# Kernel tuning notes

Hardware: AMD Instinct MI355X
Metric: run time of the kernel (lower is better)

## Reference

```python
import jax, jax.numpy as jnp
import numpy as np

C = 256
CQK = C // 8  # reduction_ratio = 8


def setup_inputs() -> dict:
    key = jax.random.key(0)
    ks = jax.random.split(key, 8)
    B, H, W = 8, 64, 64
    x = jax.random.normal(ks[0], (B, C, H, W), dtype=jnp.float32)
    s_in = 1.0 / np.sqrt(C)
    Wq = jax.random.normal(ks[1], (CQK, C), dtype=jnp.float32) * s_in
    bq = jax.random.normal(ks[2], (CQK,), dtype=jnp.float32) * 0.01
    Wk = jax.random.normal(ks[3], (CQK, C), dtype=jnp.float32) * s_in
    bk = jax.random.normal(ks[4], (CQK,), dtype=jnp.float32) * 0.01
    Wv = jax.random.normal(ks[5], (C, C), dtype=jnp.float32) * s_in
    bv = jax.random.normal(ks[6], (C,), dtype=jnp.float32) * 0.01
    gamma = jax.random.normal(ks[7], (1,), dtype=jnp.float32) * 0.1
    return {"x": x, "Wq": Wq, "bq": bq, "Wk": Wk, "bk": bk,
            "Wv": Wv, "bv": bv, "gamma": gamma}


def reference(x, Wq, bq, Wk, bk, Wv, bv, gamma):
    B, Cc, H, W = x.shape
    N = H * W
    xf = x.reshape(B, Cc, N)  # [B, C, N]
    # 1x1 convs == per-pixel linear maps over channels
    q = jnp.einsum('qc,bcn->bnq', Wq, xf) + bq            # [B, N, Cqk]
    k = jnp.einsum('kc,bcn->bkn', Wk, xf) + bk[None, :, None]  # [B, Cqk, N]
    v = jnp.einsum('vc,bcn->bvn', Wv, xf) + bv[None, :, None]  # [B, C, N]
    # unscaled attention scores, softmax over keys (last dim)
    scores = jax.nn.softmax(jnp.einsum('bnq,bqm->bnm', q, k), axis=-1)  # [B, N, N]
    # out[b,c,n] = sum_m v[b,c,m] * scores[b,n,m]  (torch: value @ scores^T)
    attn = jnp.einsum('bvm,bnm->bvn', v, scores)          # [B, C, N]
    out = gamma[0] * attn.reshape(B, Cc, H, W) + x
    return out
```

## Files before the change

### kernel.cpp

```cpp
#include <hip/hip_runtime.h>

static constexpr int B_   = 8;
static constexpr int C_   = 256;
static constexpr int CQK_ = 32;
static constexpr int N_   = 4096;

typedef __attribute__((ext_vector_type(4)))  float f32x4;
typedef __attribute__((ext_vector_type(16))) float f32x16;
typedef __attribute__((ext_vector_type(8)))  short short8;
typedef __attribute__((ext_vector_type(2)))  unsigned int u32x2;
typedef unsigned short ushort_t;

__device__ inline unsigned short f2bf(float f) {
    unsigned u = __float_as_uint(f);
    return (unsigned short)((u + 0x7FFFu + ((u >> 16) & 1u)) >> 16);
}
__device__ inline unsigned packbf(float lo, float hi) {
    return (unsigned)f2bf(lo) | ((unsigned)f2bf(hi) << 16);
}
__device__ inline unsigned cvtpk(float lo, float hi) {
    unsigned r;
    asm("v_cvt_pk_bf16_f32 %0, %1, %2" : "=v"(r) : "v"(lo), "v"(hi));
    return r;
}
__device__ inline float vexp2(float x) {
    float r;
    asm("v_exp_f32 %0, %1" : "=v"(r) : "v"(x));
    return r;
}
__device__ inline void plswap(unsigned& a, unsigned& b) {
    asm("v_permlane32_swap_b32 %0, %1" : "+v"(a), "+v"(b));
}

__device__ inline int swzbits(int m) {
    return ((m & 3) << 5) | (((m >> 3) & 1) << 4);
}

template <int OFF>
__device__ inline u32x2 tr8(unsigned a) {
    u32x2 d;
    asm volatile("ds_read_b64_tr_b16 %0, %1 offset:%2"
                 : "=v"(d) : "v"(a), "i"(OFF));
    return d;
}

__device__ inline short8 mk8(u32x2 lo, u32x2 hi) {
    union { unsigned u[4]; short8 s; } v;
    v.u[0] = lo.x; v.u[1] = lo.y; v.u[2] = hi.x; v.u[3] = hi.y;
    return v.s;
}
__device__ inline short8 mk8u(unsigned a, unsigned b, unsigned c, unsigned d) {
    union { unsigned u[4]; short8 s; } v;
    v.u[0] = a; v.u[1] = b; v.u[2] = c; v.u[3] = d;
    return v.s;
}

__global__ __launch_bounds__(256) void prep_kernel(
    const float* __restrict__ Wq, const float* __restrict__ bq,
    const float* __restrict__ Wk, const float* __restrict__ bk,
    const float* __restrict__ Wv, const float* __restrict__ bv,
    ushort_t* __restrict__ Wall, float* __restrict__ ball)
{
    const int r = blockIdx.x;
    const int t = threadIdx.x;
    const float LOG2E = 1.4426950408889634f;
    const float* src;
    float bsrc, sc;
    if (r < 32)      { src = Wq + (size_t)r * C_;        bsrc = bq[r];      sc = LOG2E; }
    else if (r < 64) { src = Wk + (size_t)(r - 32) * C_; bsrc = bk[r - 32]; sc = 1.0f; }
    else             { src = Wv + (size_t)(r - 64) * C_; bsrc = bv[r - 64]; sc = 1.0f; }
    Wall[(size_t)r * C_ + t] = f2bf(src[t] * sc);
    if (t == 0) ball[r] = bsrc * sc;
}

__global__ __launch_bounds__(256) void proj_kernel(
    const float* __restrict__ x,
    const ushort_t* __restrict__ Wall, const float* __restrict__ ball,
    ushort_t* __restrict__ Qb, ushort_t* __restrict__ Kb, ushort_t* __restrict__ Vt)
{
    __shared__ __align__(16) unsigned char xs[C_ * 128];
    typedef __attribute__((address_space(3))) unsigned char lds_byte;
    const unsigned sbase = (unsigned)(size_t)(lds_byte*)xs;

    const int b  = blockIdx.x & 7;
    const int n0 = (blockIdx.x >> 3) << 6;
    const int t  = threadIdx.x;

    {
        const int cst = t >> 4;
        const int n4  = (t & 15) << 2;
        const float* xb = x + (size_t)b * C_ * N_ + n0;
        #pragma unroll
        for (int i = 0; i < 16; ++i) {
            const int c = 16 * i + cst;
            float4 v = *(const float4*)(xb + (size_t)c * N_ + n4);
            u32x2 pk;
            pk.x = packbf(v.x, v.y);
            pk.y = packbf(v.z, v.w);
            *(u32x2*)(xs + c * 128 + ((n4 * 2) ^ swzbits(c))) = pk;
        }
    }
    __syncthreads();

    const int l  = t & 63, w = t >> 6;
    const int li = l & 15, g = l >> 4;
    const int rr = li >> 2, ss = l & 3;
    const int swz_tr = (rr << 5) | ((g & 1) << 4);

    f32x4 acc[5][4];
    #pragma unroll
    for (int i = 0; i < 5; ++i)
        #pragma unroll
        for (int j = 0; j < 4; ++j) acc[i][j] = (f32x4){0.f, 0.f, 0.f, 0.f};

    #pragma unroll 2
    for (int kg = 0; kg < 8; ++kg) {
        u32x2 pb[4][2];
        #pragma unroll
        for (int jn = 0; jn < 4; ++jn) {
            unsigned a = sbase + (32 * kg + 8 * g + rr) * 128
                       + ((32 * jn + 8 * ss) ^ swz_tr);
            pb[jn][0] = tr8<0>(a);
            pb[jn][1] = tr8<512>(a);
        }
        short8 af[5];
        #pragma unroll
        for (int tm = 0; tm < 5; ++tm)
            af[tm] = *(const short8*)(Wall + (size_t)(16 * (4 * tm + w) + li) * C_
                                      + 32 * kg + 8 * g);
        asm volatile("s_waitcnt lgkmcnt(0)" ::: "memory");
        __builtin_amdgcn_sched_barrier(0);
        #pragma unroll
        for (int jn = 0; jn < 4; ++jn) {
            short8 Bf = mk8(pb[jn][0], pb[jn][1]);
            acc[0][jn] = __builtin_amdgcn_mfma_f32_16x16x32_bf16(
                             af[0], Bf, acc[0][jn], 0, 0, 0);
            #pragma unroll
            for (int tm = 1; tm < 5; ++tm)
                acc[tm][jn] = __builtin_amdgcn_mfma_f32_16x16x32_bf16(
                                  Bf, af[tm], acc[tm][jn], 0, 0, 0);
        }
    }

    {
        const int oc0 = 16 * w + 4 * g;
        float4 bias = *(const float4*)(ball + oc0);
        ushort_t* dst = (w < 2) ? Qb : Kb;
        const int col = (w < 2) ? oc0 : (oc0 - 32);
        #pragma unroll
        for (int jn = 0; jn < 4; ++jn) {
            const int n = n0 + 16 * jn + li;
            f32x4 a = acc[0][jn];
            u32x2 pk;
            pk.x = packbf(a[0] + bias.x, a[1] + bias.y);
            pk.y = packbf(a[2] + bias.z, a[3] + bias.w);
            *(u32x2*)(dst + (size_t)(b * N_ + n) * CQK_ + col) = pk;
        }
    }
    #pragma unroll
    for (int tm = 1; tm < 5; ++tm) {
        const int c  = 16 * (4 * tm + w) + li - 64;
        const float bc = ball[64 + c];
        const int ch = c >> 7;
        const int cl = c & 127;
        const int X  = (c & 3) ^ ((c >> 2) & 3);
        char* qbase = (char*)Vt + ((size_t)(b * 64 + (n0 >> 6)) * 4 + 2 * ch) * 8192
                    + cl * 64;
        #pragma unroll
        for (int jn = 0; jn < 4; ++jn) {
            const int mp = 16 * jn + 4 * g;
            const int mh = mp >> 5;
            const int jg = (mp & 31) >> 3;
            f32x4 a = acc[tm][jn];
            u32x2 pk;
            pk.x = packbf(a[0] + bc, a[1] + bc);
            pk.y = packbf(a[2] + bc, a[3] + bc);
            *(u32x2*)(qbase + mh * 8192 + 16 * (jg ^ X) + 8 * (g & 1)) = pk;
        }
    }
}

__global__ __launch_bounds__(256, 2) void attn_kernel(
    const float* __restrict__ x,
    const ushort_t* __restrict__ Qb, const ushort_t* __restrict__ Kb,
    const ushort_t* __restrict__ Vt,
    const float* __restrict__ gamma, float* __restrict__ out)
{
    __shared__ __align__(16) unsigned char smem[66560];

    const int b   = blockIdx.x & 7;
    const int n0  = (blockIdx.x >> 3) << 6;
    const int t   = threadIdx.x;
    const int l   = t & 63, w = t >> 6;
    const int l31 = l & 31, h2 = l >> 5;
    const int mh  = w & 1,  ch = w >> 1;
    const int sxv = ((l31 & 3) ^ ((l31 >> 2) & 3)) << 4;
    unsigned char* wlds = smem + w * 16384;
    float* rstab = (float*)(smem + 65536);

    short8 qfv[2][2];
    #pragma unroll
    for (int jq = 0; jq < 2; ++jq)
        #pragma unroll
        for (int kh = 0; kh < 2; ++kh)
            qfv[jq][kh] = *(const short8*)(Qb
                + (size_t)(b * N_ + n0 + 32 * jq + l31) * CQK_ + 16 * kh + 8 * h2);

    f32x16 acc[2][4];
    #pragma unroll
    for (int i = 0; i < 2; ++i)
        #pragma unroll
        for (int j = 0; j < 4; ++j)
            #pragma unroll
            for (int e = 0; e < 16; ++e) acc[i][j][e] = 0.f;
    f32x16 zf16;
    #pragma unroll
    for (int e = 0; e < 16; ++e) zf16[e] = 0.f;
    float rs[2] = {0.f, 0.f};

    const ushort_t* Kbb = Kb + (size_t)(b * N_) * CQK_;
    const char* Vgb = (const char*)Vt + (size_t)b * 64 * 32768
                    + (2 * ch + mh) * 8192;

    short8 kfA[2], kfB[2];
    unsigned pA[2][2][4], pB[2][2][4];

#define QK_JQ(JQ, KQ, PN)                                                       \
    {                                                                           \
        f32x16 sv = __builtin_amdgcn_mfma_f32_32x32x16_bf16(                    \
                        KQ[0], qfv[JQ][0], zf16, 0, 0, 0);                      \
        sv = __builtin_amdgcn_mfma_f32_32x32x16_bf16(                           \
                 KQ[1], qfv[JQ][1], sv, 0, 0, 0);                               \
        _Pragma("unroll")                                                       \
        for (int s = 0; s < 2; ++s) {                                           \
            float e0 = vexp2(sv[8*s+0]), e1 = vexp2(sv[8*s+1]);                 \
            float e2 = vexp2(sv[8*s+2]), e3 = vexp2(sv[8*s+3]);                 \
            float e4 = vexp2(sv[8*s+4]), e5 = vexp2(sv[8*s+5]);                 \
            float e6 = vexp2(sv[8*s+6]), e7 = vexp2(sv[8*s+7]);                 \
            rs[JQ] += ((e0 + e1) + (e2 + e3)) + ((e4 + e5) + (e6 + e7));        \
            unsigned u0 = cvtpk(e0, e1), u1 = cvtpk(e2, e3);                    \
            unsigned u2 = cvtpk(e4, e5), u3 = cvtpk(e6, e7);                    \
            plswap(u0, u2); plswap(u1, u3);                                     \
            PN[JQ][s][0] = u0; PN[JQ][s][1] = u1;                               \
            PN[JQ][s][2] = u2; PN[JQ][s][3] = u3;                               \
        }                                                                       \
    }

#define PV_S(S, PC, VB)                                                         \
    {                                                                           \
        short8 A0 = mk8u(PC[0][S][0], PC[0][S][1], PC[0][S][2], PC[0][S][3]);   \
        short8 A1 = mk8u(PC[1][S][0], PC[1][S][1], PC[1][S][2], PC[1][S][3]);   \
        _Pragma("unroll")                                                       \
        for (int jc = 0; jc < 4; ++jc) {                                        \
            short8 vv = *(const short8*)((VB) + (32 * jc + l31) * 64            \
                           + ((32 * (S) + 16 * h2) ^ sxv));                     \
            acc[0][jc] = __builtin_amdgcn_mfma_f32_32x32x16_bf16(               \
                             A0, vv, acc[0][jc], 0, 0, 0);                      \
            acc[1][jc] = __builtin_amdgcn_mfma_f32_32x32x16_bf16(               \
                             A1, vv, acc[1][jc], 0, 0, 0);                      \
        }                                                                       \
    }

#define BODY(N, KQ, KL, PC, PN)                                                 \
    {                                                                           \
        const int chk = ((N) + 2) & 63;                                         \
        const int chd = ((N) + 1) & 63;                                         \
                         \
        _Pragma("unroll")                                                       \
        for (int kh = 0; kh < 2; ++kh)                                          \
            KL[kh] = *(const short8*)(Kbb                                       \
                + (size_t)(64 * chk + 32 * mh + l31) * CQK_ + 16 * kh + 8 * h2);\
                                  \
        {                                                                       \
            const char* gsrc = Vgb + (size_t)chd * 32768 + l * 16;              \
            unsigned char* ldst = wlds + (chd & 1) * 8192 + l * 16;             \
            _Pragma("unroll")                                                   \
            for (int i = 0; i < 8; ++i)                                         \
                __builtin_amdgcn_global_load_lds(                               \
                    (const __attribute__((address_space(1))) unsigned int*)(gsrc + i * 1024), \
                    (__attribute__((address_space(3))) unsigned int*)(ldst + i * 1024), \
                    16, 0, 0);                                                  \
        }                                                                       \
                \
        asm volatile("s_waitcnt vmcnt(10)" ::: "memory");                       \
                         \
        __builtin_amdgcn_s_setprio(1);                                          \
        {                                                                       \
            const unsigned char* vb = wlds + ((N) & 1) * 8192;                  \
            QK_JQ(0, KQ, PN)                                                    \
            PV_S(0, PC, vb)                                                     \
            QK_JQ(1, KQ, PN)                                                    \
            PV_S(1, PC, vb)                                                     \
        }                                                                       \
        __builtin_amdgcn_s_setprio(0);                                          \
    }

    #pragma unroll
    for (int kh = 0; kh < 2; ++kh) {
        kfA[kh] = *(const short8*)(Kbb + (size_t)(32 * mh + l31) * CQK_
                                   + 16 * kh + 8 * h2);
        kfB[kh] = *(const short8*)(Kbb + (size_t)(64 + 32 * mh + l31) * CQK_
                                   + 16 * kh + 8 * h2);
    }
    #pragma unroll
    for (int i = 0; i < 8; ++i)
        __builtin_amdgcn_global_load_lds(
            (const __attribute__((address_space(1))) unsigned int*)(Vgb + l * 16 + i * 1024),
            (__attribute__((address_space(3))) unsigned int*)(wlds + l * 16 + i * 1024),
            16, 0, 0);
    asm volatile("s_waitcnt vmcnt(10)" ::: "memory");
    QK_JQ(0, kfA, pA)
    QK_JQ(1, kfA, pA)

    for (int mc = 0; mc < 62; mc += 2) {
        BODY(mc,     kfB, kfA, pA, pB)
        BODY(mc + 1, kfA, kfB, pB, pA)
    }
    BODY(62, kfB, kfA, pA, pB)

    asm volatile("s_waitcnt vmcnt(0)" ::: "memory");
    {
        const unsigned char* vb = wlds + 8192;
        PV_S(0, pB, vb)
        PV_S(1, pB, vb)
    }
#undef BODY
#undef PV_S
#undef QK_JQ

    #pragma unroll
    for (int jq = 0; jq < 2; ++jq)
        rs[jq] += __shfl_xor(rs[jq], 32, 64);
    if (l < 32) {
        rstab[(w * 2 + 0) * 32 + l31] = rs[0];
        rstab[(w * 2 + 1) * 32 + l31] = rs[1];
    }
    __syncthreads();

    if (mh == 1) {
        float* dst = (float*)(smem + ch * 32768);
        #pragma unroll
        for (int jq = 0; jq < 2; ++jq)
            #pragma unroll
            for (int jc = 0; jc < 4; ++jc) {
                float* tb = dst + (jq * 4 + jc) * 1024 + l * 16;
                #pragma unroll
                for (int e4 = 0; e4 < 4; ++e4) {
                    f32x4 p;
                    p[0] = acc[jq][jc][4 * e4 + 0];
                    p[1] = acc[jq][jc][4 * e4 + 1];
                    p[2] = acc[jq][jc][4 * e4 + 2];
                    p[3] = acc[jq][jc][4 * e4 + 3];
                    *(f32x4*)(tb + 4 * (e4 ^ (l & 3))) = p;
                }
            }
    }
    __syncthreads();

    if (mh == 0) {
        const float* src = (const float*)(smem + ch * 32768);
        #pragma unroll
        for (int jq = 0; jq < 2; ++jq)
            #pragma unroll
            for (int jc = 0; jc < 4; ++jc) {
                const float* tb = src + (jq * 4 + jc) * 1024 + l * 16;
                #pragma unroll
                for (int e4 = 0; e4 < 4; ++e4) {
                    f32x4 p = *(const f32x4*)(tb + 4 * (e4 ^ (l & 3)));
                    acc[jq][jc][4 * e4 + 0] += p[0];
                    acc[jq][jc][4 * e4 + 1] += p[1];
                    acc[jq][jc][4 * e4 + 2] += p[2];
                    acc[jq][jc][4 * e4 + 3] += p[3];
                }
            }
        const float gm = gamma[0];
        #pragma unroll
        for (int jq = 0; jq < 2; ++jq)
            #pragma unroll
            for (int rg = 0; rg < 4; ++rg) {
                f32x4 s0 = *(const f32x4*)(rstab + (w * 2 + jq) * 32
                                           + 8 * rg + 4 * h2);
                f32x4 s1 = *(const f32x4*)(rstab + ((w + 1) * 2 + jq) * 32
                                           + 8 * rg + 4 * h2);
                float i0 = 1.0f / (s0[0] + s1[0]);
                float i1 = 1.0f / (s0[1] + s1[1]);
                float i2 = 1.0f / (s0[2] + s1[2]);
                float i3 = 1.0f / (s0[3] + s1[3]);
                const int n = n0 + 32 * jq + 8 * rg + 4 * h2;
                #pragma unroll
                for (int jc = 0; jc < 4; ++jc) {
                    const int c = 128 * ch + 32 * jc + l31;
                    const size_t rowoff = (size_t)(b * C_ + c) * N_ + n;
                    float4 xv = *(const float4*)(x + rowoff);
                    float4 o;
                    o.x = gm * acc[jq][jc][4 * rg + 0] * i0 + xv.x;
                    o.y = gm * acc[jq][jc][4 * rg + 1] * i1 + xv.y;
                    o.z = gm * acc[jq][jc][4 * rg + 2] * i2 + xv.z;
                    o.w = gm * acc[jq][jc][4 * rg + 3] * i3 + xv.w;
                    *(float4*)(out + rowoff) = o;
                }
            }
    }
}

extern "C" void kernel_launch(void* const* d_in, const int* in_sizes, int n_in,
                              void* d_out, int out_size, void* d_ws, size_t ws_size,
                              hipStream_t stream)
{
    const float* x     = (const float*)d_in[0];
    const float* Wq    = (const float*)d_in[1];
    const float* bq    = (const float*)d_in[2];
    const float* Wk    = (const float*)d_in[3];
    const float* bk    = (const float*)d_in[4];
    const float* Wv    = (const float*)d_in[5];
    const float* bv    = (const float*)d_in[6];
    const float* gamma = (const float*)d_in[7];
    float* out = (float*)d_out;

    ushort_t* ws = (ushort_t*)d_ws;
    ushort_t* Qb   = ws;
    ushort_t* Kb   = Qb + (size_t)B_ * N_ * CQK_;
    ushort_t* Vt   = Kb + (size_t)B_ * N_ * CQK_;
    ushort_t* Wall = Vt + (size_t)B_ * C_ * N_;
    float*    ball = (float*)(Wall + (size_t)320 * C_);

    prep_kernel<<<320, 256, 0, stream>>>(Wq, bq, Wk, bk, Wv, bv, Wall, ball);
    proj_kernel<<<B_ * (N_ / 64), 256, 0, stream>>>(x, Wall, ball, Qb, Kb, Vt);
    attn_kernel<<<B_ * (N_ / 64), 256, 0, stream>>>(x, Qb, Kb, Vt, gamma, out);
}
```

Measured before the change: 130.5 us.

## Split attention across channel halves, triple-buffer V, raise occupancy to three blocks

The attention grid is doubled so each block handles only 128 of the 256 output channels, which halves the accumulator registers and the V tile per block. Shared memory drops enough to target three blocks per CU, and V now uses a three-slot ring buffer with a two-chunk lookahead. The QK and exp work is also reordered ahead of the PV MFMAs inside each step. The cost is that QK^T and softmax are now computed twice per query tile, once in each channel-half block, which doubles that work and the K reads.

```diff
diff --git a/kernel.cpp b/kernel.cpp
--- a/kernel.cpp
+++ b/kernel.cpp
@@ -180,23 +180,26 @@
     }
 }
 
-__global__ __launch_bounds__(256, 2) void attn_kernel(
+__global__ __launch_bounds__(256, 3) void attn_kernel(
     const float* __restrict__ x,
     const ushort_t* __restrict__ Qb, const ushort_t* __restrict__ Kb,
     const ushort_t* __restrict__ Vt,
     const float* __restrict__ gamma, float* __restrict__ out)
 {
-    __shared__ __align__(16) unsigned char smem[66560];
-
-    const int b   = blockIdx.x & 7;
-    const int n0  = (blockIdx.x >> 3) << 6;
+    __shared__ __align__(16) unsigned char smem[50176];
+
+    const int blk = blockIdx.x;
+    const int b   = blk & 7;
+    const int nt  = (blk >> 3) & 63;
+    const int cb  = blk >> 9;
+    const int n0  = nt << 6;
     const int t   = threadIdx.x;
     const int l   = t & 63, w = t >> 6;
     const int l31 = l & 31, h2 = l >> 5;
-    const int mh  = w & 1,  ch = w >> 1;
+    const int mh  = w & 1,  ch2 = w >> 1;
     const int sxv = ((l31 & 3) ^ ((l31 >> 2) & 3)) << 4;
-    unsigned char* wlds = smem + w * 16384;
-    float* rstab = (float*)(smem + 65536);
+    unsigned char* wlds = smem + w * 12288;
+    float* rstab = (float*)(smem + 49152);
 
     short8 qfv[2][2];
     #pragma unroll
@@ -206,11 +209,11 @@
             qfv[jq][kh] = *(const short8*)(Qb
                 + (size_t)(b * N_ + n0 + 32 * jq + l31) * CQK_ + 16 * kh + 8 * h2);
 
-    f32x16 acc[2][4];
+    f32x16 acc[2][2];
     #pragma unroll
     for (int i = 0; i < 2; ++i)
         #pragma unroll
-        for (int j = 0; j < 4; ++j)
+        for (int j = 0; j < 2; ++j)
             #pragma unroll
             for (int e = 0; e < 16; ++e) acc[i][j][e] = 0.f;
     f32x16 zf16;
@@ -220,12 +223,12 @@
 
     const ushort_t* Kbb = Kb + (size_t)(b * N_) * CQK_;
     const char* Vgb = (const char*)Vt + (size_t)b * 64 * 32768
-                    + (2 * ch + mh) * 8192;
+                    + (2 * cb + mh) * 8192 + ch2 * 4096;
 
     short8 kfA[2], kfB[2];
-    unsigned pA[2][2][4], pB[2][2][4];
-
-#define QK_JQ(JQ, KQ, PN)                                                       \
+    int vcur = 0;
+
+#define QK_JQ(JQ, KQ, PAW)                                                      \
     {                                                                           \
         f32x16 sv = __builtin_amdgcn_mfma_f32_32x32x16_bf16(                    \
                         KQ[0], qfv[JQ][0], zf16, 0, 0, 0);                      \
@@ -241,58 +244,58 @@
             unsigned u0 = cvtpk(e0, e1), u1 = cvtpk(e2, e3);                    \
             unsigned u2 = cvtpk(e4, e5), u3 = cvtpk(e6, e7);                    \
             plswap(u0, u2); plswap(u1, u3);                                     \
-            PN[JQ][s][0] = u0; PN[JQ][s][1] = u1;                               \
-            PN[JQ][s][2] = u2; PN[JQ][s][3] = u3;                               \
+            PAW[JQ][s][0] = u0; PAW[JQ][s][1] = u1;                             \
+            PAW[JQ][s][2] = u2; PAW[JQ][s][3] = u3;                             \
         }                                                                       \
     }
 
-#define PV_S(S, PC, VB)                                                         \
+#define BODY(N, KC)                                                             \
     {                                                                           \
-        short8 A0 = mk8u(PC[0][S][0], PC[0][S][1], PC[0][S][2], PC[0][S][3]);   \
-        short8 A1 = mk8u(PC[1][S][0], PC[1][S][1], PC[1][S][2], PC[1][S][3]);   \
-        _Pragma("unroll")                                                       \
-        for (int jc = 0; jc < 4; ++jc) {                                        \
-            short8 vv = *(const short8*)((VB) + (32 * jc + l31) * 64            \
-                           + ((32 * (S) + 16 * h2) ^ sxv));                     \
-            acc[0][jc] = __builtin_amdgcn_mfma_f32_32x32x16_bf16(               \
-                             A0, vv, acc[0][jc], 0, 0, 0);                      \
-            acc[1][jc] = __builtin_amdgcn_mfma_f32_32x32x16_bf16(               \
-                             A1, vv, acc[1][jc], 0, 0, 0);                      \
-        }                                                                       \
-    }
-
-#define BODY(N, KQ, KL, PC, PN)                                                 \
-    {                                                                           \
-        const int chk = ((N) + 2) & 63;                                         \
-        const int chd = ((N) + 1) & 63;                                         \
-                         \
-        _Pragma("unroll")                                                       \
-        for (int kh = 0; kh < 2; ++kh)                                          \
-            KL[kh] = *(const short8*)(Kbb                                       \
-                + (size_t)(64 * chk + 32 * mh + l31) * CQK_ + 16 * kh + 8 * h2);\
-                                  \
+        const int chd = ((N) + 2) & 63;                                         \
+                                \
+        int vnext = vcur + 2; if (vnext >= 3) vnext -= 3;                       \
         {                                                                       \
             const char* gsrc = Vgb + (size_t)chd * 32768 + l * 16;              \
-            unsigned char* ldst = wlds + (chd & 1) * 8192 + l * 16;             \
+            unsigned char* ldst = wlds + vnext * 4096 + l * 16;                 \
             _Pragma("unroll")                                                   \
-            for (int i = 0; i < 8; ++i)                                         \
+            for (int i = 0; i < 4; ++i)                                         \
                 __builtin_amdgcn_global_load_lds(                               \
                     (const __attribute__((address_space(1))) unsigned int*)(gsrc + i * 1024), \
                     (__attribute__((address_space(3))) unsigned int*)(ldst + i * 1024), \
                     16, 0, 0);                                                  \
         }                                                                       \
-                \
-        asm volatile("s_waitcnt vmcnt(10)" ::: "memory");                       \
-                         \
-        __builtin_amdgcn_s_setprio(1);                                          \
+                                      \
+        unsigned paw[2][2][4];                                                  \
+        QK_JQ(0, KC, paw)                                                       \
+        QK_JQ(1, KC, paw)                                                       \
+                                      \
+        _Pragma("unroll")                                                       \
+        for (int kh = 0; kh < 2; ++kh)                                          \
+            KC[kh] = *(const short8*)(Kbb                                       \
+                + (size_t)(64 * chd + 32 * mh + l31) * CQK_ + 16 * kh + 8 * h2);\
+                     \
+        asm volatile("s_waitcnt vmcnt(12)" ::: "memory");                       \
+                            \
         {                                                                       \
-            const unsigned char* vb = wlds + ((N) & 1) * 8192;                  \
-            QK_JQ(0, KQ, PN)                                                    \
-            PV_S(0, PC, vb)                                                     \
-            QK_JQ(1, KQ, PN)                                                    \
-            PV_S(1, PC, vb)                                                     \
+            const unsigned char* vb = wlds + vcur * 4096;                       \
+            _Pragma("unroll")                                                   \
+            for (int s = 0; s < 2; ++s) {                                       \
+                short8 A0 = mk8u(paw[0][s][0], paw[0][s][1],                    \
+                                 paw[0][s][2], paw[0][s][3]);                   \
+                short8 A1 = mk8u(paw[1][s][0], paw[1][s][1],                    \
+                                 paw[1][s][2], paw[1][s][3]);                   \
+                _Pragma("unroll")                                               \
+                for (int jc = 0; jc < 2; ++jc) {                                \
+                    short8 vv = *(const short8*)(vb + (32 * jc + l31) * 64      \
+                                   + ((32 * s + 16 * h2) ^ sxv));               \
+                    acc[0][jc] = __builtin_amdgcn_mfma_f32_32x32x16_bf16(       \
+                                     A0, vv, acc[0][jc], 0, 0, 0);              \
+                    acc[1][jc] = __builtin_amdgcn_mfma_f32_32x32x16_bf16(       \
+                                     A1, vv, acc[1][jc], 0, 0, 0);              \
+                }                                                               \
+            }                                                                   \
         }                                                                       \
-        __builtin_amdgcn_s_setprio(0);                                          \
+        vcur = (vcur == 2) ? 0 : vcur + 1;                                      \
     }
 
     #pragma unroll
@@ -303,29 +306,45 @@
                                    + 16 * kh + 8 * h2);
     }
     #pragma unroll
-    for (int i = 0; i < 8; ++i)
+    for (int i = 0; i < 4; ++i) {
         __builtin_amdgcn_global_load_lds(
             (const __attribute__((address_space(1))) unsigned int*)(Vgb + l * 16 + i * 1024),
             (__attribute__((address_space(3))) unsigned int*)(wlds + l * 16 + i * 1024),
             16, 0, 0);
-    asm volatile("s_waitcnt vmcnt(10)" ::: "memory");
-    QK_JQ(0, kfA, pA)
-    QK_JQ(1, kfA, pA)
+        __builtin_amdgcn_global_load_lds(
+            (const __attribute__((address_space(1))) unsigned int*)(Vgb + 32768 + l * 16 + i * 1024),
+            (__attribute__((address_space(3))) unsigned int*)(wlds + 4096 + l * 16 + i * 1024),
+            16, 0, 0);
+    }
 
     for (int mc = 0; mc < 62; mc += 2) {
-        BODY(mc,     kfB, kfA, pA, pB)
-        BODY(mc + 1, kfA, kfB, pB, pA)
-    }
-    BODY(62, kfB, kfA, pA, pB)
-
-    asm volatile("s_waitcnt vmcnt(0)" ::: "memory");
+        BODY(mc,     kfA)
+        BODY(mc + 1, kfB)
+    }
+    BODY(62, kfA)
+
     {
-        const unsigned char* vb = wlds + 8192;
-        PV_S(0, pB, vb)
-        PV_S(1, pB, vb)
+        unsigned paw[2][2][4];
+        QK_JQ(0, kfB, paw)
+        QK_JQ(1, kfB, paw)
+        asm volatile("s_waitcnt vmcnt(0)" ::: "memory");
+        const unsigned char* vb = wlds + vcur * 4096;
+        #pragma unroll
+        for (int s = 0; s < 2; ++s) {
+            short8 A0 = mk8u(paw[0][s][0], paw[0][s][1], paw[0][s][2], paw[0][s][3]);
+            short8 A1 = mk8u(paw[1][s][0], paw[1][s][1], paw[1][s][2], paw[1][s][3]);
+            #pragma unroll
+            for (int jc = 0; jc < 2; ++jc) {
+                short8 vv = *(const short8*)(vb + (32 * jc + l31) * 64
+                               + ((32 * s + 16 * h2) ^ sxv));
+                acc[0][jc] = __builtin_amdgcn_mfma_f32_32x32x16_bf16(
+                                 A0, vv, acc[0][jc], 0, 0, 0);
+                acc[1][jc] = __builtin_amdgcn_mfma_f32_32x32x16_bf16(
+                                 A1, vv, acc[1][jc], 0, 0, 0);
+            }
+        }
     }
 #undef BODY
-#undef PV_S
 #undef QK_JQ
 
     #pragma unroll
@@ -338,12 +357,12 @@
     __syncthreads();
 
     if (mh == 1) {
-        float* dst = (float*)(smem + ch * 32768);
+        float* dst = (float*)(smem + ch2 * 16384);
         #pragma unroll
         for (int jq = 0; jq < 2; ++jq)
             #pragma unroll
-            for (int jc = 0; jc < 4; ++jc) {
-                float* tb = dst + (jq * 4 + jc) * 1024 + l * 16;
+            for (int jc = 0; jc < 2; ++jc) {
+                float* tb = dst + (jq * 2 + jc) * 1024 + l * 16;
                 #pragma unroll
                 for (int e4 = 0; e4 < 4; ++e4) {
                     f32x4 p;
@@ -358,12 +377,12 @@
     __syncthreads();
 
     if (mh == 0) {
-        const float* src = (const float*)(smem + ch * 32768);
+        const float* src = (const float*)(smem + ch2 * 16384);
         #pragma unroll
         for (int jq = 0; jq < 2; ++jq)
             #pragma unroll
-            for (int jc = 0; jc < 4; ++jc) {
-                const float* tb = src + (jq * 4 + jc) * 1024 + l * 16;
+            for (int jc = 0; jc < 2; ++jc) {
+                const float* tb = src + (jq * 2 + jc) * 1024 + l * 16;
                 #pragma unroll
                 for (int e4 = 0; e4 < 4; ++e4) {
                     f32x4 p = *(const f32x4*)(tb + 4 * (e4 ^ (l & 3)));
@@ -388,8 +407,8 @@
                 float i3 = 1.0f / (s0[3] + s1[3]);
                 const int n = n0 + 32 * jq + 8 * rg + 4 * h2;
                 #pragma unroll
-                for (int jc = 0; jc < 4; ++jc) {
-                    const int c = 128 * ch + 32 * jc + l31;
+                for (int jc = 0; jc < 2; ++jc) {
+                    const int c = 128 * cb + 64 * ch2 + 32 * jc + l31;
                     const size_t rowoff = (size_t)(b * C_ + c) * N_ + n;
                     float4 xv = *(const float4*)(x + rowoff);
                     float4 o;
@@ -426,5 +445,5 @@
 
     prep_kernel<<<320, 256, 0, stream>>>(Wq, bq, Wk, bk, Wv, bv, Wall, ball);
     proj_kernel<<<B_ * (N_ / 64), 256, 0, stream>>>(x, Wall, ball, Qb, Kb, Vt);
-    attn_kernel<<<B_ * (N_ / 64), 256, 0, stream>>>(x, Qb, Kb, Vt, gamma, out);
-}
+    attn_kernel<<<B_ * (N_ / 64) * 2, 256, 0, stream>>>(x, Qb, Kb, Vt, gamma, out);
+}
```

New measurement: 245.3 us. +88.0%, slower.

## Split key chunks across two wave groups in 512-thread attention blocks

Applied to the files above, without the earlier changes.

The attention kernel moves from 256 to 512 threads per block. Each pair of waves now takes alternating key chunks (even or odd) with a single-buffered per-wave V tile in LDS, replacing the software-pipelined double-buffered loop. The partial accumulators and row sums are merged through LDS in a multi-stage reduction at the end. This exposes more waves per CU to hide latency, at the cost of losing the explicit QK/PV pipelining, adding extra barriers and reduction traffic, and possibly lowering occupancy because launch_bounds(256,2) was dropped.

```diff
diff --git a/kernel.cpp b/kernel.cpp
--- a/kernel.cpp
+++ b/kernel.cpp
@@ -180,22 +180,24 @@
     }
 }
 
-__global__ __launch_bounds__(256, 2) void attn_kernel(
+__global__ __launch_bounds__(512) void attn_kernel(
     const float* __restrict__ x,
     const ushort_t* __restrict__ Qb, const ushort_t* __restrict__ Kb,
     const ushort_t* __restrict__ Vt,
     const float* __restrict__ gamma, float* __restrict__ out)
 {
-    __shared__ __align__(16) unsigned char smem[66560];
+    __shared__ __align__(16) unsigned char smem[67584];
 
     const int b   = blockIdx.x & 7;
     const int n0  = (blockIdx.x >> 3) << 6;
     const int t   = threadIdx.x;
     const int l   = t & 63, w = t >> 6;
     const int l31 = l & 31, h2 = l >> 5;
-    const int mh  = w & 1,  ch = w >> 1;
+    const int g   = w & 1;
+    const int mh  = (w >> 1) & 1;
+    const int ch2 = w >> 2;
     const int sxv = ((l31 & 3) ^ ((l31 >> 2) & 3)) << 4;
-    unsigned char* wlds = smem + w * 16384;
+    unsigned char* wlds = smem + w * 8192;
     float* rstab = (float*)(smem + 65536);
 
     short8 qfv[2][2];
@@ -220,17 +222,16 @@
 
     const ushort_t* Kbb = Kb + (size_t)(b * N_) * CQK_;
     const char* Vgb = (const char*)Vt + (size_t)b * 64 * 32768
-                    + (2 * ch + mh) * 8192;
-
-    short8 kfA[2], kfB[2];
-    unsigned pA[2][2][4], pB[2][2][4];
-
-#define QK_JQ(JQ, KQ, PN)                                                       \
+                    + (2 * ch2 + mh) * 8192;
+
+    short8 kf[2];
+
+#define QK_JQ(JQ, PAW)                                                          \
     {                                                                           \
         f32x16 sv = __builtin_amdgcn_mfma_f32_32x32x16_bf16(                    \
-                        KQ[0], qfv[JQ][0], zf16, 0, 0, 0);                      \
+                        kf[0], qfv[JQ][0], zf16, 0, 0, 0);                      \
         sv = __builtin_amdgcn_mfma_f32_32x32x16_bf16(                           \
-                 KQ[1], qfv[JQ][1], sv, 0, 0, 0);                               \
+                 kf[1], qfv[JQ][1], sv, 0, 0, 0);                               \
         _Pragma("unroll")                                                       \
         for (int s = 0; s < 2; ++s) {                                           \
             float e0 = vexp2(sv[8*s+0]), e1 = vexp2(sv[8*s+1]);                 \
@@ -241,109 +242,84 @@
             unsigned u0 = cvtpk(e0, e1), u1 = cvtpk(e2, e3);                    \
             unsigned u2 = cvtpk(e4, e5), u3 = cvtpk(e6, e7);                    \
             plswap(u0, u2); plswap(u1, u3);                                     \
-            PN[JQ][s][0] = u0; PN[JQ][s][1] = u1;                               \
-            PN[JQ][s][2] = u2; PN[JQ][s][3] = u3;                               \
+            PAW[JQ][s][0] = u0; PAW[JQ][s][1] = u1;                             \
+            PAW[JQ][s][2] = u2; PAW[JQ][s][3] = u3;                             \
         }                                                                       \
     }
 
-#define PV_S(S, PC, VB)                                                         \
-    {                                                                           \
-        short8 A0 = mk8u(PC[0][S][0], PC[0][S][1], PC[0][S][2], PC[0][S][3]);   \
-        short8 A1 = mk8u(PC[1][S][0], PC[1][S][1], PC[1][S][2], PC[1][S][3]);   \
-        _Pragma("unroll")                                                       \
-        for (int jc = 0; jc < 4; ++jc) {                                        \
-            short8 vv = *(const short8*)((VB) + (32 * jc + l31) * 64            \
-                           + ((32 * (S) + 16 * h2) ^ sxv));                     \
-            acc[0][jc] = __builtin_amdgcn_mfma_f32_32x32x16_bf16(               \
-                             A0, vv, acc[0][jc], 0, 0, 0);                      \
-            acc[1][jc] = __builtin_amdgcn_mfma_f32_32x32x16_bf16(               \
-                             A1, vv, acc[1][jc], 0, 0, 0);                      \
-        }                                                                       \
-    }
-
-#define BODY(N, KQ, KL, PC, PN)                                                 \
-    {                                                                           \
-        const int chk = ((N) + 2) & 63;                                         \
-        const int chd = ((N) + 1) & 63;                                         \
-                         \
-        _Pragma("unroll")                                                       \
-        for (int kh = 0; kh < 2; ++kh)                                          \
-            KL[kh] = *(const short8*)(Kbb                                       \
-                + (size_t)(64 * chk + 32 * mh + l31) * CQK_ + 16 * kh + 8 * h2);\
-                                  \
-        {                                                                       \
-            const char* gsrc = Vgb + (size_t)chd * 32768 + l * 16;              \
-            unsigned char* ldst = wlds + (chd & 1) * 8192 + l * 16;             \
-            _Pragma("unroll")                                                   \
-            for (int i = 0; i < 8; ++i)                                         \
-                __builtin_amdgcn_global_load_lds(                               \
-                    (const __attribute__((address_space(1))) unsigned int*)(gsrc + i * 1024), \
-                    (__attribute__((address_space(3))) unsigned int*)(ldst + i * 1024), \
-                    16, 0, 0);                                                  \
-        }                                                                       \
-                \
-        asm volatile("s_waitcnt vmcnt(10)" ::: "memory");                       \
-                         \
-        __builtin_amdgcn_s_setprio(1);                                          \
-        {                                                                       \
-            const unsigned char* vb = wlds + ((N) & 1) * 8192;                  \
-            QK_JQ(0, KQ, PN)                                                    \
-            PV_S(0, PC, vb)                                                     \
-            QK_JQ(1, KQ, PN)                                                    \
-            PV_S(1, PC, vb)                                                     \
-        }                                                                       \
-        __builtin_amdgcn_s_setprio(0);                                          \
-    }
-
-    #pragma unroll
-    for (int kh = 0; kh < 2; ++kh) {
-        kfA[kh] = *(const short8*)(Kbb + (size_t)(32 * mh + l31) * CQK_
-                                   + 16 * kh + 8 * h2);
-        kfB[kh] = *(const short8*)(Kbb + (size_t)(64 + 32 * mh + l31) * CQK_
-                                   + 16 * kh + 8 * h2);
-    }
+    #pragma unroll
+    for (int kh = 0; kh < 2; ++kh)
+        kf[kh] = *(const short8*)(Kbb + (size_t)(64 * g + 32 * mh + l31) * CQK_
+                                  + 16 * kh + 8 * h2);
     #pragma unroll
     for (int i = 0; i < 8; ++i)
         __builtin_amdgcn_global_load_lds(
-            (const __attribute__((address_space(1))) unsigned int*)(Vgb + l * 16 + i * 1024),
+            (const __attribute__((address_space(1))) unsigned int*)
+                (Vgb + (size_t)g * 32768 + l * 16 + i * 1024),
             (__attribute__((address_space(3))) unsigned int*)(wlds + l * 16 + i * 1024),
             16, 0, 0);
-    asm volatile("s_waitcnt vmcnt(10)" ::: "memory");
-    QK_JQ(0, kfA, pA)
-    QK_JQ(1, kfA, pA)
-
-    for (int mc = 0; mc < 62; mc += 2) {
-        BODY(mc,     kfB, kfA, pA, pB)
-        BODY(mc + 1, kfA, kfB, pB, pA)
-    }
-    BODY(62, kfB, kfA, pA, pB)
+
+    for (int i = 0; i < 32; ++i) {
+        const int n = g + 2 * i;
+        unsigned paw[2][2][4];
+        QK_JQ(0, paw)
+        QK_JQ(1, paw)
+        {
+            const int chk = (n + 2) & 63;
+            #pragma unroll
+            for (int kh = 0; kh < 2; ++kh)
+                kf[kh] = *(const short8*)(Kbb
+                    + (size_t)(64 * chk + 32 * mh + l31) * CQK_ + 16 * kh + 8 * h2);
+        }
+        asm volatile("s_waitcnt vmcnt(2)" ::: "memory");
+        __builtin_amdgcn_s_setprio(1);
+        #pragma unroll
+        for (int s = 0; s < 2; ++s) {
+            short8 A0 = mk8u(paw[0][s][0], paw[0][s][1], paw[0][s][2], paw[0][s][3]);
+            short8 A1 = mk8u(paw[1][s][0], paw[1][s][1], paw[1][s][2], paw[1][s][3]);
+            #pragma unroll
+            for (int jc = 0; jc < 4; ++jc) {
+                short8 vv = *(const short8*)(wlds + (32 * jc + l31) * 64
+                               + ((32 * s + 16 * h2) ^ sxv));
+                acc[0][jc] = __builtin_amdgcn_mfma_f32_32x32x16_bf16(
+                                 A0, vv, acc[0][jc], 0, 0, 0);
+                acc[1][jc] = __builtin_amdgcn_mfma_f32_32x32x16_bf16(
+                                 A1, vv, acc[1][jc], 0, 0, 0);
+            }
+        }
+        __builtin_amdgcn_s_setprio(0);
+        asm volatile("s_waitcnt lgkmcnt(0)" ::: "memory");
+        {
+            const int chd = (n + 2) & 63;
+            const char* gsrc = Vgb + (size_t)chd * 32768 + l * 16;
+            #pragma unroll
+            for (int i2 = 0; i2 < 8; ++i2)
+                __builtin_amdgcn_global_load_lds(
+                    (const __attribute__((address_space(1))) unsigned int*)(gsrc + i2 * 1024),
+                    (__attribute__((address_space(3))) unsigned int*)(wlds + l * 16 + i2 * 1024),
+                    16, 0, 0);
+        }
+    }
+#undef QK_JQ
 
     asm volatile("s_waitcnt vmcnt(0)" ::: "memory");
-    {
-        const unsigned char* vb = wlds + 8192;
-        PV_S(0, pB, vb)
-        PV_S(1, pB, vb)
-    }
-#undef BODY
-#undef PV_S
-#undef QK_JQ
 
     #pragma unroll
     for (int jq = 0; jq < 2; ++jq)
         rs[jq] += __shfl_xor(rs[jq], 32, 64);
     if (l < 32) {
-        rstab[(w * 2 + 0) * 32 + l31] = rs[0];
-        rstab[(w * 2 + 1) * 32 + l31] = rs[1];
-    }
-    __syncthreads();
-
-    if (mh == 1) {
-        float* dst = (float*)(smem + ch * 32768);
-        #pragma unroll
-        for (int jq = 0; jq < 2; ++jq)
-            #pragma unroll
-            for (int jc = 0; jc < 4; ++jc) {
-                float* tb = dst + (jq * 4 + jc) * 1024 + l * 16;
+        rstab[w * 64 + l31]      = rs[0];
+        rstab[w * 64 + 32 + l31] = rs[1];
+    }
+
+    const float gm = gamma[0];
+    #pragma unroll
+    for (int jq = 0; jq < 2; ++jq) {
+        __syncthreads();
+        if (g == 1) {
+            float* tb = (float*)(smem + (2 * mh + ch2) * 16384);
+            #pragma unroll
+            for (int jc = 0; jc < 4; ++jc)
                 #pragma unroll
                 for (int e4 = 0; e4 < 4; ++e4) {
                     f32x4 p;
@@ -351,45 +327,65 @@
                     p[1] = acc[jq][jc][4 * e4 + 1];
                     p[2] = acc[jq][jc][4 * e4 + 2];
                     p[3] = acc[jq][jc][4 * e4 + 3];
-                    *(f32x4*)(tb + 4 * (e4 ^ (l & 3))) = p;
+                    *(f32x4*)(tb + jc * 1024 + l * 16 + 4 * (e4 ^ (l & 3))) = p;
                 }
-            }
-    }
-    __syncthreads();
-
-    if (mh == 0) {
-        const float* src = (const float*)(smem + ch * 32768);
-        #pragma unroll
-        for (int jq = 0; jq < 2; ++jq)
-            #pragma unroll
-            for (int jc = 0; jc < 4; ++jc) {
-                const float* tb = src + (jq * 4 + jc) * 1024 + l * 16;
+        }
+        __syncthreads();
+        if (g == 0) {
+            const float* tb = (const float*)(smem + (2 * mh + ch2) * 16384);
+            #pragma unroll
+            for (int jc = 0; jc < 4; ++jc)
                 #pragma unroll
                 for (int e4 = 0; e4 < 4; ++e4) {
-                    f32x4 p = *(const f32x4*)(tb + 4 * (e4 ^ (l & 3)));
+                    f32x4 p = *(const f32x4*)(tb + jc * 1024 + l * 16 + 4 * (e4 ^ (l & 3)));
                     acc[jq][jc][4 * e4 + 0] += p[0];
                     acc[jq][jc][4 * e4 + 1] += p[1];
                     acc[jq][jc][4 * e4 + 2] += p[2];
                     acc[jq][jc][4 * e4 + 3] += p[3];
                 }
-            }
-        const float gm = gamma[0];
-        #pragma unroll
-        for (int jq = 0; jq < 2; ++jq)
+        }
+        __syncthreads();
+        if (g == 0 && mh == 1) {
+            float* tb = (float*)(smem + ch2 * 16384);
+            #pragma unroll
+            for (int jc = 0; jc < 4; ++jc)
+                #pragma unroll
+                for (int e4 = 0; e4 < 4; ++e4) {
+                    f32x4 p;
+                    p[0] = acc[jq][jc][4 * e4 + 0];
+                    p[1] = acc[jq][jc][4 * e4 + 1];
+                    p[2] = acc[jq][jc][4 * e4 + 2];
+                    p[3] = acc[jq][jc][4 * e4 + 3];
+                    *(f32x4*)(tb + jc * 1024 + l * 16 + 4 * (e4 ^ (l & 3))) = p;
+                }
+        }
+        __syncthreads();
+        if (g == 0 && mh == 0) {
+            const float* tb = (const float*)(smem + ch2 * 16384);
+            #pragma unroll
+            for (int jc = 0; jc < 4; ++jc)
+                #pragma unroll
+                for (int e4 = 0; e4 < 4; ++e4) {
+                    f32x4 p = *(const f32x4*)(tb + jc * 1024 + l * 16 + 4 * (e4 ^ (l & 3)));
+                    acc[jq][jc][4 * e4 + 0] += p[0];
+                    acc[jq][jc][4 * e4 + 1] += p[1];
+                    acc[jq][jc][4 * e4 + 2] += p[2];
+                    acc[jq][jc][4 * e4 + 3] += p[3];
+                }
             #pragma unroll
             for (int rg = 0; rg < 4; ++rg) {
-                f32x4 s0 = *(const f32x4*)(rstab + (w * 2 + jq) * 32
-                                           + 8 * rg + 4 * h2);
-                f32x4 s1 = *(const f32x4*)(rstab + ((w + 1) * 2 + jq) * 32
-                                           + 8 * rg + 4 * h2);
-                float i0 = 1.0f / (s0[0] + s1[0]);
-                float i1 = 1.0f / (s0[1] + s1[1]);
-                float i2 = 1.0f / (s0[2] + s1[2]);
-                float i3 = 1.0f / (s0[3] + s1[3]);
+                const int ro = 32 * jq + 8 * rg + 4 * h2;
+                f32x4 s0 = *(const f32x4*)(rstab + (4 * ch2 + 0) * 64 + ro);
+                f32x4 s1 = *(const f32x4*)(rstab + (4 * ch2 + 1) * 64 + ro);
+                f32x4 s2 = *(const f32x4*)(rstab + (4 * ch2 + 2) * 64 + ro);
+                f32x4 s3 = *(const f32x4*)(rstab + (4 * ch2 + 3) * 64 + ro);
+                f32x4 sm = (s0 + s1) + (s2 + s3);
+                float i0 = 1.0f / sm[0], i1 = 1.0f / sm[1];
+                float i2 = 1.0f / sm[2], i3 = 1.0f / sm[3];
                 const int n = n0 + 32 * jq + 8 * rg + 4 * h2;
                 #pragma unroll
                 for (int jc = 0; jc < 4; ++jc) {
-                    const int c = 128 * ch + 32 * jc + l31;
+                    const int c = 128 * ch2 + 32 * jc + l31;
                     const size_t rowoff = (size_t)(b * C_ + c) * N_ + n;
                     float4 xv = *(const float4*)(x + rowoff);
                     float4 o;
@@ -400,6 +396,7 @@
                     *(float4*)(out + rowoff) = o;
                 }
             }
+        }
     }
 }
 
@@ -426,5 +423,5 @@
 
     prep_kernel<<<320, 256, 0, stream>>>(Wq, bq, Wk, bk, Wv, bv, Wall, ball);
     proj_kernel<<<B_ * (N_ / 64), 256, 0, stream>>>(x, Wall, ball, Qb, Kb, Vt);
-    attn_kernel<<<B_ * (N_ / 64), 256, 0, stream>>>(x, Qb, Kb, Vt, gamma, out);
-}
+    attn_kernel<<<B_ * (N_ / 64), 512, 0, stream>>>(x, Qb, Kb, Vt, gamma, out);
+}
```

New measurement: 136.3 us. 1.04x slower.
